# Optimization experiments

Hardware: AMD Instinct MI355X
Metric: run time of the kernel (lower is better)

## Reference

```python
import jax, jax.numpy as jnp
import numpy as np

LO = 1e-5      # probability floor, matches ctc_align_targets lo=1e-05
SKIP = -5.0    # skip penalty, matches forward_algorithm default


def log_add(x, y):
    # Faithful translation of the numpy log_add (piecewise-stable logaddexp variant).
    return jnp.where(jnp.abs(x - y) > 10,
                     jnp.maximum(x, y),
                     jnp.log(jnp.exp(jnp.clip(x - y, -20, 20)) + 1) + y)


def forward_final(lmatch):
    """Forward DP over an (S, T) log-match matrix; returns the final state vector v (T,).
    Matches forward_algorithm: v_i = log_add(v + m_i, roll(v,1)[0:=skip*i] + m_i)."""
    S, T = lmatch.shape
    v0 = SKIP * jnp.arange(T, dtype=lmatch.dtype)

    def step(v, mi):
        m, i = mi
        w = jnp.roll(v, 1).at[0].set(SKIP * i)
        v = log_add(v + m, w + m)
        return v, None

    idx = jnp.arange(S, dtype=lmatch.dtype)
    v_last, _ = jax.lax.scan(step, v0, (lmatch, idx))
    return v_last


def make_targets_onehot(labels, n_classes):
    """labels: (L, N) int -> (2L+1, N, C) blank-interleaved one-hot targets.
    Row layout: blank, l_0, blank, l_1, ..., blank, l_{L-1}, blank."""
    L, N = labels.shape
    padded = jnp.zeros((2 * L + 1, N), dtype=labels.dtype)
    padded = padded.at[1::2].set(labels)  # rows 1,3,...,2L-1
    return jax.nn.one_hot(padded, n_classes, dtype=jnp.float32)


def ctc_loss_single(out, tgt):
    # out: (S, C) network outputs; tgt: (T, C) one-hot target states
    out = jnp.maximum(LO, out)
    out = out / jnp.sum(out, axis=1, keepdims=True)
    lmatch = jnp.log(out @ tgt.T)        # (S, T)
    v = forward_final(lmatch)            # (T,)
    return -log_add(v[-1], v[-2])


def setup_inputs() -> dict:
    key = jax.random.key(0)
    k1, k2 = jax.random.split(key)
    S, N, C, L = 1024, 32, 128, 128
    inp = jax.random.uniform(k1, (S, N, C), dtype=jnp.float32)
    targets = jax.random.randint(k2, (L, N), 0, C, dtype=jnp.int64)
    return {"input": inp, "targets": targets}


def reference(input, targets):
    S, N, C = input.shape
    onehot = make_targets_onehot(targets, C)                     # (T, N, C)
    losses = jax.vmap(ctc_loss_single, in_axes=(1, 1))(input, onehot)  # (N,)
    # reduce=True, size_average=True: sum over batch then divide by N
    return jnp.sum(losses) / N
```

## Files before the change

kernel.cpp:

```cpp
#include <hip/hip_runtime.h>
#include <hip/hip_bf16.h>


#define S_LEN 1024
#define N_B   32
#define C_CLS 128
#define LOV   1e-5f
#define L2E   7.213475f
#define E_M5  6.7379470e-03f
#define LN2   0.69314718f

#define ROW_B 640
#define PFD   16

typedef unsigned int  u32;
typedef unsigned short u16;

__device__ __forceinline__ u32 bf16r(float x) {
    u32 u = __builtin_bit_cast(u32, x);
    return (u + 0x7FFFu + ((u >> 16) & 1u)) >> 16;
}
__device__ __forceinline__ float bf_lo(u32 w) {
    return __builtin_bit_cast(float, w << 16);
}
__device__ __forceinline__ float bf_hi(u32 w) {
    return __builtin_bit_cast(float, w & 0xFFFF0000u);
}

__device__ __forceinline__ int shl1_i(int x, bool row0lane) {
    int a = __builtin_amdgcn_update_dpp(0, x, 0x111, 0xf, 0xf, false);
    int b = __builtin_amdgcn_update_dpp(0, x, 0x142, 0xf, 0xf, false);
    return row0lane ? b : a;
}
__device__ __forceinline__ float shl1_f(float x, bool row0lane) {
    return __builtin_bit_cast(float, shl1_i(__builtin_bit_cast(int, x), row0lane));
}

__global__ void __launch_bounds__(256)
ctc_pre_kernel(const float* __restrict__ inp, const int* __restrict__ lab,
               unsigned char* __restrict__ g, int chunk_start, int ch) {
    __shared__ float lp[4][C_CLS];
    const int wid  = threadIdx.x >> 6;
    const int lane = threadIdx.x & 63;
    const int W = blockIdx.x * 4 + wid;
    const int n  = W & 31;
    const int sb = (W >> 5) * 8;

    int offs[5];
    #pragma unroll
    for (int j = 0; j < 5; ++j) {
        int t = 5 * lane + j;
        int c = 0;
        if (t & 1) { int idx = (t - 1) >> 1; if (idx > 127) idx = 127; c = lab[idx * N_B + n]; }
        offs[j] = c << 2;
    }

    for (int r = 0; r < 8; ++r) {
        const int sl = sb + r;
        const int s  = chunk_start + sl;
        const float* row = inp + ((size_t)s * N_B + n) * C_CLS;
        float2 x = *(const float2*)(row + 2 * lane);
        float p0 = fmaxf(LOV, x.x), p1 = fmaxf(LOV, x.y);
        float sum = p0 + p1;
        #pragma unroll
        for (int off = 32; off; off >>= 1) sum += __shfl_xor(sum, off);
        float rinv = 1.0f / sum;
        float2 q2; q2.x = p0 * rinv; q2.y = p1 * rinv;
        *(float2*)&lp[wid][2 * lane] = q2;
        const char* lpb = (const char*)&lp[wid][0];
        float g0 = *(const float*)(lpb + offs[0]);
        float g1 = *(const float*)(lpb + offs[1]);
        float g2 = *(const float*)(lpb + offs[2]);
        float g3 = *(const float*)(lpb + offs[3]);
        float g4 = *(const float*)(lpb + offs[4]);
        unsigned char* orow = g + ((size_t)n * ch + sl) * ROW_B;
        *(u32*)(orow + 4 * lane)       = bf16r(g0) | (bf16r(g1) << 16);
        *(u32*)(orow + 256 + 4 * lane) = bf16r(g2) | (bf16r(g3) << 16);
        *(u16*)(orow + 512 + 2 * lane) = (u16)bf16r(g4);
    }
}

__global__ void __launch_bounds__(64)
ctc_dp_kernel(const unsigned char* __restrict__ g,
              float* __restrict__ vst,
              float* __restrict__ losses,
              int chunk_start, int ch, int is_last) {
    const int n = blockIdx.x;
    const int lane = threadIdx.x;
    const bool row0lane = (lane & 15) == 0;
    const bool lane0 = (lane == 0);

    float u0, u1, u2, u3, u4; int ref;
    float* vr = vst + ((size_t)n * 64 + lane) * 6;
    if (chunk_start == 0) {
        ref = (int)(-36.067375f * (float)lane);
        u0 = exp2f(fmaf(-L2E, (float)(5 * lane + 0), -(float)ref));
        u1 = exp2f(fmaf(-L2E, (float)(5 * lane + 1), -(float)ref));
        u2 = exp2f(fmaf(-L2E, (float)(5 * lane + 2), -(float)ref));
        u3 = exp2f(fmaf(-L2E, (float)(5 * lane + 3), -(float)ref));
        u4 = exp2f(fmaf(-L2E, (float)(5 * lane + 4), -(float)ref));
    } else {
        u0 = vr[0]; u1 = vr[1]; u2 = vr[2]; u3 = vr[3]; u4 = vr[4];
        ref = __builtin_bit_cast(int, vr[5]);
    }

    const unsigned char* gn = g + (size_t)n * ch * ROW_B;
    const int oA = 4 * lane, oB = 256 + 4 * lane, oC = 512 + 2 * lane;

    u32 pfA[PFD], pfB[PFD], pfC[PFD];
    #pragma unroll
    for (int k = 0; k < PFD; ++k) {
        const unsigned char* rp = gn + (size_t)k * ROW_B;
        pfA[k] = *(const u32*)(rp + oA);
        pfB[k] = *(const u32*)(rp + oB);
        pfC[k] = *(const u16*)(rp + oC);
    }

    const int nblk = ch >> 4;
    for (int blk = 0; blk < nblk; ++blk) {
        const int i0 = blk << 4;
        #pragma unroll
        for (int q4 = 0; q4 < 4; ++q4) {
            int refL = shl1_i(ref, row0lane);
            float fct = ldexpf(1.0f, refL - ref);
            float prev0 = exp2f(fmaf(-L2E, (float)(chunk_start + i0 + 4 * q4),
                                     -(float)ref));
            #pragma unroll
            for (int k = 0; k < 4; ++k) {
                const int slot = q4 * 4 + k;
                const int i = i0 + slot;
                float cq0 = bf_lo(pfA[slot]), cq1 = bf_hi(pfA[slot]);
                float cq2 = bf_lo(pfB[slot]), cq3 = bf_hi(pfB[slot]);
                float cq4 = __builtin_bit_cast(float, pfC[slot] << 16);
                int sp = i + PFD; if (sp > ch - 1) sp = ch - 1;
                const unsigned char* rp = gn + (size_t)sp * ROW_B;
                pfA[slot] = *(const u32*)(rp + oA);
                pfB[slot] = *(const u32*)(rp + oB);
                pfC[slot] = *(const u16*)(rp + oC);
                float u4s  = shl1_f(u4, row0lane);
                float prev = lane0 ? prev0 : u4s * fct;
                float w0 = cq0 * (u0 + prev);
                float w1 = cq1 * (u1 + u0);
                float w2 = cq2 * (u2 + u1);
                float w3 = cq3 * (u3 + u2);
                float w4 = cq4 * (u4 + u3);
                u0 = w0; u1 = w1; u2 = w2; u3 = w3; u4 = w4;
                prev0 *= E_M5;
            }
            float M = fmaxf(fmaxf(fmaxf(u0, u1), fmaxf(u2, u3)), u4);
            int e = ((__builtin_bit_cast(int, M) >> 23) & 255) - 126;
            ref += e;
            u0 = ldexpf(u0, -e); u1 = ldexpf(u1, -e); u2 = ldexpf(u2, -e);
            u3 = ldexpf(u3, -e); u4 = ldexpf(u4, -e);
        }
    }

    if (!is_last) {
        vr[0] = u0; vr[1] = u1; vr[2] = u2; vr[3] = u3; vr[4] = u4;
        vr[5] = __builtin_bit_cast(float, ref);
    } else if (lane == 51) {
        losses[n] = -(LN2 * (float)ref + __logf(u0 + u1));
    }
}

__global__ void ctc_sum_kernel(const float* __restrict__ losses,
                               float* __restrict__ out) {
    const int lane = threadIdx.x;
    float x = (lane < N_B) ? losses[lane] : 0.0f;
    #pragma unroll
    for (int off = 32; off; off >>= 1) x += __shfl_xor(x, off);
    if (lane == 0) out[0] = x / (float)N_B;
}

extern "C" void kernel_launch(void* const* d_in, const int* in_sizes, int n_in,
                              void* d_out, int out_size, void* d_ws, size_t ws_size,
                              hipStream_t stream) {
    const float* inp = (const float*)d_in[0];
    const int*   lab = (const int*)d_in[1];
    float* out = (float*)d_out;

    char* ws = (char*)d_ws;
    const size_t V_BYTES = (size_t)N_B * 64 * 6 * 4;
    const size_t L_OFF = V_BYTES;
    const size_t M_OFF = (L_OFF + N_B * 4 + 511) & ~(size_t)511;
    float* vst    = (float*)ws;
    float* losses = (float*)(ws + L_OFF);
    unsigned char* mbuf = (unsigned char*)(ws + M_OFF);

    size_t usable = (ws_size > M_OFF) ? (ws_size - M_OFF) : 0;
    int CH = (int)(usable / ((size_t)N_B * ROW_B));
    CH &= ~127;
    if (CH > S_LEN) CH = S_LEN;
    if (CH < 128) CH = 128;

    for (int cs = 0; cs < S_LEN; cs += CH) {
        int ch = S_LEN - cs; if (ch > CH) ch = CH;
        ctc_pre_kernel<<<ch, 256, 0, stream>>>(inp, lab, mbuf, cs, ch);
        ctc_dp_kernel<<<N_B, 64, 0, stream>>>(mbuf, vst, losses,
                                              cs, ch, (cs + ch >= S_LEN) ? 1 : 0);
    }
    ctc_sum_kernel<<<1, 64, 0, stream>>>(losses, out);
}
```

Measured before the change: 165.7 us.

## Store match probabilities as fp32 in 4-step groups with asm-pipelined dwordx4 loads

```diff
diff --git a/kernel.cpp b/kernel.cpp
--- a/kernel.cpp
+++ b/kernel.cpp
@@ -10,22 +10,8 @@
 #define E_M5  6.7379470e-03f
 #define LN2   0.69314718f
 
-#define ROW_B 640
-#define PFD   16
-
-typedef unsigned int  u32;
-typedef unsigned short u16;
-
-__device__ __forceinline__ u32 bf16r(float x) {
-    u32 u = __builtin_bit_cast(u32, x);
-    return (u + 0x7FFFu + ((u >> 16) & 1u)) >> 16;
-}
-__device__ __forceinline__ float bf_lo(u32 w) {
-    return __builtin_bit_cast(float, w << 16);
-}
-__device__ __forceinline__ float bf_hi(u32 w) {
-    return __builtin_bit_cast(float, w & 0xFFFF0000u);
-}
+#define GRP_B  5120
+#define G_PIPE 8
 
 __device__ __forceinline__ int shl1_i(int x, bool row0lane) {
     int a = __builtin_amdgcn_update_dpp(0, x, 0x111, 0xf, 0xf, false);
@@ -36,15 +22,32 @@
     return __builtin_bit_cast(float, shl1_i(__builtin_bit_cast(int, x), row0lane));
 }
 
+#define ISSUE_GROUP(sidx, rp)                                                  \
+    do {                                                                       \
+        const char* _rp = (rp);                                                \
+        const char* _rpC = _rp + 4096;                                         \
+        asm volatile(                                                          \
+            "global_load_dwordx4 %0, %5, %6 offset:0\n\t"                      \
+            "global_load_dwordx4 %1, %5, %6 offset:1024\n\t"                   \
+            "global_load_dwordx4 %2, %5, %6 offset:2048\n\t"                   \
+            "global_load_dwordx4 %3, %5, %6 offset:3072\n\t"                   \
+            "global_load_dwordx4 %4, %5, %7 offset:0"                          \
+            : "=v"(A1[sidx]), "=v"(A2[sidx]), "=v"(B1[sidx]),                  \
+              "=v"(B2[sidx]), "=v"(C4[sidx])                                   \
+            : "v"(lane16), "s"(_rp), "s"(_rpC)                                 \
+            : "memory");                                                       \
+    } while (0)
+
 __global__ void __launch_bounds__(256)
 ctc_pre_kernel(const float* __restrict__ inp, const int* __restrict__ lab,
-               unsigned char* __restrict__ g, int chunk_start, int ch) {
+               float* __restrict__ gbuf, int chunk_start, int ch) {
     __shared__ float lp[4][C_CLS];
     const int wid  = threadIdx.x >> 6;
     const int lane = threadIdx.x & 63;
-    const int W = blockIdx.x * 4 + wid;
-    const int n  = W & 31;
-    const int sb = (W >> 5) * 8;
+    const int R = blockIdx.x * 4 + wid;
+    const int n  = R & 31;
+    const int sl = R >> 5;
+    const int s  = chunk_start + sl;
 
     int offs[5];
     #pragma unroll
@@ -55,33 +58,31 @@
         offs[j] = c << 2;
     }
 
-    for (int r = 0; r < 8; ++r) {
-        const int sl = sb + r;
-        const int s  = chunk_start + sl;
-        const float* row = inp + ((size_t)s * N_B + n) * C_CLS;
-        float2 x = *(const float2*)(row + 2 * lane);
-        float p0 = fmaxf(LOV, x.x), p1 = fmaxf(LOV, x.y);
-        float sum = p0 + p1;
-        #pragma unroll
-        for (int off = 32; off; off >>= 1) sum += __shfl_xor(sum, off);
-        float rinv = 1.0f / sum;
-        float2 q2; q2.x = p0 * rinv; q2.y = p1 * rinv;
-        *(float2*)&lp[wid][2 * lane] = q2;
-        const char* lpb = (const char*)&lp[wid][0];
-        float g0 = *(const float*)(lpb + offs[0]);
-        float g1 = *(const float*)(lpb + offs[1]);
-        float g2 = *(const float*)(lpb + offs[2]);
-        float g3 = *(const float*)(lpb + offs[3]);
-        float g4 = *(const float*)(lpb + offs[4]);
-        unsigned char* orow = g + ((size_t)n * ch + sl) * ROW_B;
-        *(u32*)(orow + 4 * lane)       = bf16r(g0) | (bf16r(g1) << 16);
-        *(u32*)(orow + 256 + 4 * lane) = bf16r(g2) | (bf16r(g3) << 16);
-        *(u16*)(orow + 512 + 2 * lane) = (u16)bf16r(g4);
-    }
+    const float* row = inp + ((size_t)s * N_B + n) * C_CLS;
+    float2 x = *(const float2*)(row + 2 * lane);
+    float p0 = fmaxf(LOV, x.x), p1 = fmaxf(LOV, x.y);
+    float sum = p0 + p1;
+    #pragma unroll
+    for (int off = 32; off; off >>= 1) sum += __shfl_xor(sum, off);
+    float rinv = 1.0f / sum;
+    *(float2*)&lp[wid][2 * lane] = make_float2(p0 * rinv, p1 * rinv);
+    const char* lpb = (const char*)&lp[wid][0];
+    float g0 = *(const float*)(lpb + offs[0]);
+    float g1 = *(const float*)(lpb + offs[1]);
+    float g2 = *(const float*)(lpb + offs[2]);
+    float g3 = *(const float*)(lpb + offs[3]);
+    float g4 = *(const float*)(lpb + offs[4]);
+
+    const int g = sl >> 2, k = sl & 3;
+    float* base = gbuf + ((size_t)n * (ch >> 2) + g) * (GRP_B / 4);
+    const int half = (k >> 1) * 256, odd = (k & 1) * 2;
+    *(float2*)(base + half + lane * 4 + odd)       = make_float2(g0, g1);
+    *(float2*)(base + 512 + half + lane * 4 + odd) = make_float2(g2, g3);
+    base[1024 + lane * 4 + k] = g4;
 }
 
 __global__ void __launch_bounds__(64)
-ctc_dp_kernel(const unsigned char* __restrict__ g,
+ctc_dp_kernel(const float* __restrict__ gbuf,
               float* __restrict__ vst,
               float* __restrict__ losses,
               int chunk_start, int ch, int is_last) {
@@ -89,6 +90,7 @@
     const int lane = threadIdx.x;
     const bool row0lane = (lane & 15) == 0;
     const bool lane0 = (lane == 0);
+    const unsigned lane16 = lane * 16;
 
     float u0, u1, u2, u3, u4; int ref;
     float* vr = vst + ((size_t)n * 64 + lane) * 6;
@@ -104,39 +106,35 @@
         ref = __builtin_bit_cast(int, vr[5]);
     }
 
-    const unsigned char* gn = g + (size_t)n * ch * ROW_B;
-    const int oA = 4 * lane, oB = 256 + 4 * lane, oC = 512 + 2 * lane;
-
-    u32 pfA[PFD], pfB[PFD], pfC[PFD];
-    #pragma unroll
-    for (int k = 0; k < PFD; ++k) {
-        const unsigned char* rp = gn + (size_t)k * ROW_B;
-        pfA[k] = *(const u32*)(rp + oA);
-        pfB[k] = *(const u32*)(rp + oB);
-        pfC[k] = *(const u16*)(rp + oC);
-    }
-
-    const int nblk = ch >> 4;
-    for (int blk = 0; blk < nblk; ++blk) {
-        const int i0 = blk << 4;
+    const int ng = ch >> 2;
+    const char* nbase = (const char*)(gbuf + (size_t)n * ng * (GRP_B / 4));
+
+    float4 A1[G_PIPE], A2[G_PIPE], B1[G_PIPE], B2[G_PIPE], C4[G_PIPE];
+
+    #pragma unroll
+    for (int sidx = 0; sidx < G_PIPE; ++sidx)
+        ISSUE_GROUP(sidx, nbase + (size_t)sidx * GRP_B);
+
+    for (int g0 = 0; g0 < ng; g0 += G_PIPE) {
         #pragma unroll
-        for (int q4 = 0; q4 < 4; ++q4) {
+        for (int sidx = 0; sidx < G_PIPE; ++sidx) {
+            const int g = g0 + sidx;
+            asm volatile("s_waitcnt vmcnt(35)" ::: "memory");
+            __builtin_amdgcn_sched_barrier(0);
+            float4 a1 = A1[sidx], a2 = A2[sidx];
+            float4 b1 = B1[sidx], b2 = B2[sidx], c4 = C4[sidx];
+
             int refL = shl1_i(ref, row0lane);
             float fct = ldexpf(1.0f, refL - ref);
-            float prev0 = exp2f(fmaf(-L2E, (float)(chunk_start + i0 + 4 * q4),
+            float prev0 = exp2f(fmaf(-L2E, (float)(chunk_start + 4 * g),
                                      -(float)ref));
             #pragma unroll
             for (int k = 0; k < 4; ++k) {
-                const int slot = q4 * 4 + k;
-                const int i = i0 + slot;
-                float cq0 = bf_lo(pfA[slot]), cq1 = bf_hi(pfA[slot]);
-                float cq2 = bf_lo(pfB[slot]), cq3 = bf_hi(pfB[slot]);
-                float cq4 = __builtin_bit_cast(float, pfC[slot] << 16);
-                int sp = i + PFD; if (sp > ch - 1) sp = ch - 1;
-                const unsigned char* rp = gn + (size_t)sp * ROW_B;
-                pfA[slot] = *(const u32*)(rp + oA);
-                pfB[slot] = *(const u32*)(rp + oB);
-                pfC[slot] = *(const u16*)(rp + oC);
+                float cq0, cq1, cq2, cq3, cq4;
+                if (k == 0)      { cq0=a1.x; cq1=a1.y; cq2=b1.x; cq3=b1.y; cq4=c4.x; }
+                else if (k == 1) { cq0=a1.z; cq1=a1.w; cq2=b1.z; cq3=b1.w; cq4=c4.y; }
+                else if (k == 2) { cq0=a2.x; cq1=a2.y; cq2=b2.x; cq3=b2.y; cq4=c4.z; }
+                else             { cq0=a2.z; cq1=a2.w; cq2=b2.z; cq3=b2.w; cq4=c4.w; }
                 float u4s  = shl1_f(u4, row0lane);
                 float prev = lane0 ? prev0 : u4s * fct;
                 float w0 = cq0 * (u0 + prev);
@@ -152,8 +150,12 @@
             ref += e;
             u0 = ldexpf(u0, -e); u1 = ldexpf(u1, -e); u2 = ldexpf(u2, -e);
             u3 = ldexpf(u3, -e); u4 = ldexpf(u4, -e);
+
+            int sp = g + G_PIPE; if (sp > ng - 1) sp = ng - 1;
+            ISSUE_GROUP(sidx, nbase + (size_t)sp * GRP_B);
         }
     }
+    asm volatile("s_waitcnt vmcnt(0)" ::: "memory");
 
     if (!is_last) {
         vr[0] = u0; vr[1] = u1; vr[2] = u2; vr[3] = u3; vr[4] = u4;
@@ -185,17 +187,17 @@
     const size_t M_OFF = (L_OFF + N_B * 4 + 511) & ~(size_t)511;
     float* vst    = (float*)ws;
     float* losses = (float*)(ws + L_OFF);
-    unsigned char* mbuf = (unsigned char*)(ws + M_OFF);
+    float* mbuf   = (float*)(ws + M_OFF);
 
     size_t usable = (ws_size > M_OFF) ? (ws_size - M_OFF) : 0;
-    int CH = (int)(usable / ((size_t)N_B * ROW_B));
+    int CH = (int)(usable / ((size_t)N_B * (GRP_B / 4)));
     CH &= ~127;
     if (CH > S_LEN) CH = S_LEN;
     if (CH < 128) CH = 128;
 
     for (int cs = 0; cs < S_LEN; cs += CH) {
         int ch = S_LEN - cs; if (ch > CH) ch = CH;
-        ctc_pre_kernel<<<ch, 256, 0, stream>>>(inp, lab, mbuf, cs, ch);
+        ctc_pre_kernel<<<ch * N_B / 4, 256, 0, stream>>>(inp, lab, mbuf, cs, ch);
         ctc_dp_kernel<<<N_B, 64, 0, stream>>>(mbuf, vst, losses,
                                               cs, ch, (cs + ch >= S_LEN) ? 1 : 0);
     }
```

Result: faster. 144.9 us (-12.6%).
